# Kernel tuning notes

Hardware: AMD Instinct MI355X
Metric: run time of the kernel (lower is better)

## Reference

```python
import jax, jax.numpy as jnp
import numpy as np

D0, D1 = 512, 512          # PSF / sensor dims (DIMS0, DIMS1)
P0, P1 = D0 // 2, D1 // 2  # pad sizes
ITERS = 20
MU1, MU2, MU3 = 1e-6, 1e-5, 1e-5
TAU = 1e-4 * 1000.0        # 0.1, as in module


def _ct(x):  # zero-pad crop-adjoint: sensor -> full size
    return jnp.pad(x, [(0, 0)] * (x.ndim - 2) + [(P0, P0), (P1, P1)])


def _c(x):  # crop full -> sensor size
    return x[..., P0:P0 + D0, P1:P1 + D1]


def _fft2(x):
    return jnp.fft.fft2(x, axes=(-2, -1))


def _ifft2(x):
    return jnp.fft.ifft2(x, axes=(-2, -1))


def _ifftshift(x):
    return jnp.fft.ifftshift(x, axes=(-2, -1))


def _fftshift(x):
    return jnp.fft.fftshift(x, axes=(-2, -1))


def _H(x, Hf):  # forward blur operator
    return jnp.real(_fftshift(_ifft2(Hf * _fft2(_ifftshift(x)))))


def _Hadj(x, Hf):  # adjoint blur operator
    return jnp.real(_fftshift(_ifft2(jnp.conj(Hf) * _fft2(_ifftshift(x)))))


def _psi(x):  # finite differences stacked on last axis -> (..., 2)
    return jnp.stack([jnp.roll(x, 1, axis=-2) - x,
                      jnp.roll(x, 1, axis=-1) - x], axis=-1)


def _psit(u):  # adjoint of _psi
    d0, d1 = u[..., 0], u[..., 1]
    return (jnp.roll(d0, -1, axis=-2) - d0) + (jnp.roll(d1, -1, axis=-1) - d1)


def _soft(v, thresh):
    return jnp.sign(v) * jnp.maximum(jnp.abs(v) - thresh, 0.0)


def _make_ltl():  # FFT of laplacian kernel (Psi^T Psi in Fourier domain)
    lapl = np.zeros((2 * D0, 2 * D1), np.float32)
    lapl[0, 0] = 4.0
    lapl[0, 1] = -1.0
    lapl[1, 0] = -1.0
    lapl[0, -1] = -1.0
    lapl[-1, 0] = -1.0
    return jnp.fft.fft2(jnp.asarray(lapl))


def setup_inputs() -> dict:
    key = jax.random.key(0)
    k1, k2 = jax.random.split(key)
    y = jax.random.uniform(k1, (8, 1, D0, D1), dtype=jnp.float32)
    h = jax.random.uniform(k2, (D0, D1), dtype=jnp.float32)
    return {"y": y, "h": h}


def reference(y, h):
    Hf = _fft2(_ifftshift(_ct(h[None])))            # (1, 2D0, 2D1) complex
    LtL = _make_ltl()                               # (2D0, 2D1) complex
    Vdiv = 1.0 / (_ct(jnp.ones((1, 1, D0, D1), y.dtype)) + MU1)
    Rdiv = 1.0 / (MU1 * jnp.abs(jnp.conj(Hf) * Hf) + MU2 * jnp.abs(LtL) + MU3)
    CTy = _ct(y)                                    # (B,1,2D0,2D1)

    B = y.shape[0]
    full = (B, 1, 2 * D0, 2 * D1)
    X = jnp.zeros(full, y.dtype)
    U = jnp.zeros(full + (2,), y.dtype)
    V = jnp.zeros(full, y.dtype)
    W = jnp.zeros(full, y.dtype)
    a1 = jnp.zeros(full, y.dtype)
    a2 = jnp.zeros(full + (2,), y.dtype)
    a3 = jnp.zeros(full, y.dtype)

    def step(carry, _):
        X, U, V, W, a1, a2, a3 = carry
        U = _soft(_psi(X) + a2 / MU2, TAU / MU2)
        V = Vdiv * (a1 + MU1 * _H(X, Hf) + CTy)
        W = jnp.maximum(a3 / MU3 + X, 0.0)
        r = (MU3 * W - a3) + _psit(MU2 * U - a2) + _Hadj(MU1 * V - a1, Hf)
        X = jnp.real(_fftshift(_ifft2(Rdiv * _fft2(_ifftshift(r)))))
        a1 = a1 + MU1 * (_H(X, Hf) - V)
        a2 = a2 + MU2 * (_psi(X) - U)
        a3 = a3 + MU3 * (X - W)
        return (X, U, V, W, a1, a2, a3), None

    (X, _, _, _, _, _, _), _ = jax.lax.scan(step, (X, U, V, W, a1, a2, a3), None, length=ITERS)
    return _c(X)
```

## Files before the change

kernel.cpp:

```cpp
#include <hip/hip_runtime.h>
#include <math.h>

#define N 1024
#define NN (1024*1024)
#define BATCH 8

static constexpr float MU1 = 1e-6f, MU2 = 1e-5f, MU3 = 1e-5f;

__device__ __forceinline__ float2 cmulf(float2 a, float2 b){
  return make_float2(a.x*b.x - a.y*b.y, a.x*b.y + a.y*b.x);
}
__device__ __forceinline__ float2 conjf(float2 a){ return make_float2(a.x, -a.y); }
__device__ __forceinline__ float softf(float v, float T){
  float a = fmaxf(fabsf(v) - T, 0.f);
  return copysignf(a, v);
}
__device__ __forceinline__ int rev4_10(int p){
  return ((p&3)<<8) | (((p>>2)&3)<<6) | (((p>>4)&3)<<4) | (((p>>6)&3)<<2) | ((p>>8)&3);
}
__device__ __forceinline__ int foldc(int k){
  if (k == 0) return 0;
  if (k == 512) return 1;
  return (k < 512) ? 2*k : 2*(1024-k)+1;
}
__device__ __forceinline__ int unfoldc(int c){
  if (c < 2) return c ? 512 : 0;
  return (c & 1) ? 1024 - ((c-1)>>1) : (c>>1);
}

#define BF4F(x0,x1,x2,x3,u0,u1,u2,u3) { \
  float2 t02p = make_float2((x0).x+(x2).x, (x0).y+(x2).y); \
  float2 t02m = make_float2((x0).x-(x2).x, (x0).y-(x2).y); \
  float2 t13p = make_float2((x1).x+(x3).x, (x1).y+(x3).y); \
  float2 t13m = make_float2((x1).x-(x3).x, (x1).y-(x3).y); \
  u0 = make_float2(t02p.x+t13p.x, t02p.y+t13p.y); \
  u2 = make_float2(t02p.x-t13p.x, t02p.y-t13p.y); \
  u1 = make_float2(t02m.x+t13m.y, t02m.y-t13m.x); \
  u3 = make_float2(t02m.x-t13m.y, t02m.y+t13m.x); }
#define BF4I(x0,x1,x2,x3,u0,u1,u2,u3) { \
  float2 t02p = make_float2((x0).x+(x2).x, (x0).y+(x2).y); \
  float2 t02m = make_float2((x0).x-(x2).x, (x0).y-(x2).y); \
  float2 t13p = make_float2((x1).x+(x3).x, (x1).y+(x3).y); \
  float2 t13m = make_float2((x1).x-(x3).x, (x1).y-(x3).y); \
  u0 = make_float2(t02p.x+t13p.x, t02p.y+t13p.y); \
  u2 = make_float2(t02p.x-t13p.x, t02p.y-t13p.y); \
  u1 = make_float2(t02m.x-t13m.y, t02m.y+t13m.x); \
  u3 = make_float2(t02m.x+t13m.y, t02m.y-t13m.x); }

template<int DIR>
__device__ __forceinline__ void fft1024(float2* bufA, float2* bufB,
                                        const float2* Ws, int tid){
  float2* cur = bufA; float2* oth = bufB;
  int s = 1;
  for (int st = 0; st < 10; ++st){
    int m = 512 >> st;
    #pragma unroll
    for (int bb = 0; bb < 2; ++bb){
      int b = tid + bb*256;
      int p = b >> st;
      int q = b & (s-1);
      float2 a = cur[b];
      float2 c = cur[b + 512];
      float2 w = Ws[b & ~(s-1)];
      if (DIR > 0) w.y = -w.y;
      float2 d = make_float2(a.x - c.x, a.y - c.y);
      oth[q + s*(2*p)]   = make_float2(a.x + c.x, a.y + c.y);
      oth[q + s*(2*p+1)] = cmulf(d, w);
    }
    __syncthreads();
    float2* t = cur; cur = oth; oth = t;
    s <<= 1;
  }
}

__global__ void k_twiddle(float2* W){
  int j = blockIdx.x*blockDim.x + threadIdx.x;
  if (j < 768){
    double a = -2.0 * M_PI * (double)j / 1024.0;
    W[j] = make_float2((float)cos(a), (float)sin(a));
  }
}

__global__ void k_build_h(const float* __restrict__ h, float2* __restrict__ Z){
  int idx = blockIdx.x*256 + threadIdx.x;
  int i = idx >> 10, j = idx & 1023;
  float v = 0.f;
  if (i >= 256 && i < 768 && j >= 256 && j < 768)
    v = h[(i-256)*512 + (j-256)];
  Z[idx] = make_float2(v, 0.f);
}

__global__ void k_filters2(const float2* __restrict__ ZT, float2* __restrict__ HfCb,
                           float* __restrict__ RdCb){
  int id = blockIdx.x*256 + threadIdx.x;
  int blk = id >> 13;
  int rem = id & 8191;
  int p = rem >> 3, c = rem & 7;
  int colp = (blk << 3) | c;
  int ki = rev4_10(p);
  int kj = unfoldc(colp);
  float2 v = ZT[((size_t)kj << 10) | (size_t)ki];
  float sgn = ((ki + kj) & 1) ? -1.f : 1.f;
  HfCb[id] = make_float2(sgn*v.x, sgn*v.y);
  double mag2 = (double)v.x*(double)v.x + (double)v.y*(double)v.y;
  double ltl = 4.0 - 2.0*cos(2.0*M_PI*(double)ki/1024.0)
                   - 2.0*cos(2.0*M_PI*(double)kj/1024.0);
  double rd = 1.0 / ((double)MU1*mag2 + (double)MU2*ltl + (double)MU3);
  RdCb[id] = (float)(rd / ((double)N * (double)N));
}

__global__ void k_init(float* __restrict__ X, float* __restrict__ G1,
                       float* __restrict__ K, float* __restrict__ M,
                       float* __restrict__ G0a, float* __restrict__ G0b,
                       const float* __restrict__ y){
  int idx = blockIdx.x*256 + threadIdx.x;
  int e = idx >> 20, r = (idx >> 10) & 1023, c = idx & 1023;
  X[idx] = 0.f; G1[idx] = 0.f; K[idx] = 0.f; G0a[idx] = 0.f; G0b[idx] = 0.f;
  float m = 0.f;
  if (r >= 256 && r < 768 && c >= 256 && c < 768)
    m = y[(size_t)e*262144 + (size_t)(r-256)*512 + (c-256)] * (MU1/(1.f + MU1));
  M[idx] = m;
}

__global__ __launch_bounds__(256) void k_pA(const float* __restrict__ X,
                                            const float* __restrict__ G0r,
                                            float* __restrict__ G0w,
                                            const float* __restrict__ G1,
                                            const float* __restrict__ K,
                                            const float* __restrict__ M,
                                            float2* __restrict__ Z,
                                            const float2* __restrict__ Wg, int e0){
  __shared__ float2 bufA[N], bufB[N], Ws[512];
  int tid = threadIdx.x;
  int bid = blockIdx.x;
  int i = ((bid & 7) << 7) + (bid >> 3);
  int ce = blockIdx.y, e = e0 + ce;
  size_t eb  = (size_t)e*NN;
  size_t rb  = eb + (size_t)i*N;
  size_t rbm = eb + (size_t)((i-1)&1023)*N;
  size_t rbp = eb + (size_t)((i+1)&1023)*N;
  size_t zb  = (size_t)ce*NN + (size_t)i*N;
  for (int k = tid; k < 512; k += 256) Ws[k] = Wg[k];
  const float T = 1e4f;
  for (int j = tid; j < N; j += 256){
    float xm = X[rbm+j], x = X[rb+j], xp = X[rbp+j];
    float psi0  = xm - x;
    float psi0p = x - xp;
    float g0  = G0r[rb+j], g0p = G0r[rbp+j];
    float u0  = softf(2.f*psi0  - g0 *(1.f/MU2), T);
    float u0p = softf(2.f*psi0p - g0p*(1.f/MU2), T);
    float g0n  = MU2*(u0  - psi0 ) + g0;
    float g0np = MU2*(u0p - psi0p) + g0p;
    G0w[rb+j] = g0n;
    int jp = (j+1) & 1023;
    float s = K[rb+j] + (g0np - g0n) + (G1[rb+jp] - G1[rb+j]);
    bufA[j] = make_float2(s, M[rb+j]);
  }
  __syncthreads();
  fft1024<-1>(bufA, bufB, Ws, tid);
  for (int j = tid; j < N; j += 256) bufB[foldc(j)] = bufA[j];
  __syncthreads();
  for (int j = tid; j < N; j += 256) Z[zb+j] = bufB[j];
}

template<int DIR>
__global__ __launch_bounds__(256) void k_fft_row(float2* Z, const float2* __restrict__ Wg){
  __shared__ float2 bufA[N], bufB[N], Ws[512];
  int tid = threadIdx.x;
  size_t base = ((size_t)blockIdx.y * N + blockIdx.x) * N;
  for (int k = tid; k < 512; k += 256) Ws[k] = Wg[k];
  for (int k = tid; k < N; k += 256) bufA[k] = Z[base + k];
  __syncthreads();
  fft1024<DIR>(bufA, bufB, Ws, tid);
  for (int k = tid; k < N; k += 256) Z[base + k] = bufA[k];
}

__global__ void k_transpose_ip(float2* Z){
  __shared__ float2 ta[32][33], tb[32][33];
  int t = blockIdx.x, ti = 0;
  while (t >= 32 - ti){ t -= 32 - ti; ti++; }
  int tj = ti + t;
  size_t base = (size_t)blockIdx.y * NN;
  int ra = ti*32, ca = tj*32;
  for (int k = threadIdx.y; k < 32; k += 8){
    ta[k][threadIdx.x] = Z[base + (size_t)(ra+k)*N + ca + threadIdx.x];
    if (ti != tj)
      tb[k][threadIdx.x] = Z[base + (size_t)(ca+k)*N + ra + threadIdx.x];
  }
  __syncthreads();
  for (int k = threadIdx.y; k < 32; k += 8){
    Z[base + (size_t)(ra+k)*N + ca + threadIdx.x] = (ti!=tj) ? tb[threadIdx.x][k]
                                                             : ta[threadIdx.x][k];
    if (ti != tj)
      Z[base + (size_t)(ca+k)*N + ra + threadIdx.x] = ta[threadIdx.x][k];
  }
}

#define TADDR(r,c) ((((r)*9) + (c)) ^ (((r) & 16) >> 1))
#define CPV 512
__global__ __launch_bounds__(CPV, 4) void k_colpass(float2* __restrict__ Z,
    const float2* __restrict__ HfCb, const float* __restrict__ RdCb,
    const float2* __restrict__ Wg){
  __shared__ float2 tile[9216];
  __shared__ float2 Ws[768];
  int tid = threadIdx.x;
  int blk = blockIdx.x;
  size_t zbase = (size_t)blockIdx.y*NN + ((size_t)blk<<3);
  for (int k = tid; k < 768; k += CPV) Ws[k] = Wg[k];
  for (int k = tid; k < 8192; k += CPV){
    int r = k >> 3, c = k & 7;
    tile[TADDR(r,c)] = Z[zbase + (size_t)r*N + c];
  }
  __syncthreads();
  {
    int c = tid & 7, j2 = tid >> 3;
    float2 v[4][4];
    #pragma unroll
    for (int a = 0; a < 4; ++a)
      #pragma unroll
      for (int b = 0; b < 4; ++b)
        v[a][b] = tile[TADDR(j2 + 64*b + 256*a, c)];
    #pragma unroll
    for (int b = 0; b < 4; ++b){
      int j1 = j2 + 64*b;
      float2 u0,u1,u2,u3;
      BF4F(v[0][b],v[1][b],v[2][b],v[3][b],u0,u1,u2,u3);
      v[0][b] = u0;
      v[1][b] = cmulf(u1, Ws[j1]);
      v[2][b] = cmulf(u2, Ws[2*j1]);
      v[3][b] = cmulf(u3, Ws[3*j1]);
    }
    int tw = j2 << 2;
    #pragma unroll
    for (int a = 0; a < 4; ++a){
      float2 u0,u1,u2,u3;
      BF4F(v[a][0],v[a][1],v[a][2],v[a][3],u0,u1,u2,u3);
      tile[TADDR(j2 + 256*a, c)]       = u0;
      tile[TADDR(j2 + 64 + 256*a, c)]  = cmulf(u1, Ws[tw]);
      tile[TADDR(j2 + 128 + 256*a, c)] = cmulf(u2, Ws[2*tw]);
      tile[TADDR(j2 + 192 + 256*a, c)] = cmulf(u3, Ws[3*tw]);
    }
  }
  __syncthreads();
  {
    int c = tid & 7, vv = tid >> 3;
    int B2 = vv >> 2, j2 = vv & 3;
    int r0 = 64*B2 + j2;
    float2 v[4][4];
    #pragma unroll
    for (int a = 0; a < 4; ++a)
      #pragma unroll
      for (int b = 0; b < 4; ++b)
        v[a][b] = tile[TADDR(r0 + 4*b + 16*a, c)];
    #pragma unroll
    for (int b = 0; b < 4; ++b){
      int tw = (j2 + 4*b) << 4;
      float2 u0,u1,u2,u3;
      BF4F(v[0][b],v[1][b],v[2][b],v[3][b],u0,u1,u2,u3);
      v[0][b] = u0;
      v[1][b] = cmulf(u1, Ws[tw]);
      v[2][b] = cmulf(u2, Ws[2*tw]);
      v[3][b] = cmulf(u3, Ws[3*tw]);
    }
    int tw3 = j2 << 6;
    #pragma unroll
    for (int a = 0; a < 4; ++a){
      float2 u0,u1,u2,u3;
      BF4F(v[a][0],v[a][1],v[a][2],v[a][3],u0,u1,u2,u3);
      tile[TADDR(r0 + 16*a, c)]      = u0;
      tile[TADDR(r0 + 16*a + 4, c)]  = cmulf(u1, Ws[tw3]);
      tile[TADDR(r0 + 16*a + 8, c)]  = cmulf(u2, Ws[2*tw3]);
      tile[TADDR(r0 + 16*a + 12, c)] = cmulf(u3, Ws[3*tw3]);
    }
  }
  __syncthreads();
  for (int k = tid; k < 2048; k += CPV){
    int c = k & 7, t = k >> 3;
    int r = 4*t;
    float2 x0 = tile[TADDR(r,c)],   x1 = tile[TADDR(r+1,c)];
    float2 x2 = tile[TADDR(r+2,c)], x3 = tile[TADDR(r+3,c)];
    float2 u0,u1,u2,u3;
    BF4F(x0,x1,x2,x3,u0,u1,u2,u3);
    tile[TADDR(r,c)] = u0; tile[TADDR(r+1,c)] = u1;
    tile[TADDR(r+2,c)] = u2; tile[TADDR(r+3,c)] = u3;
  }
  __syncthreads();
  {
    size_t fbase = (size_t)blk << 13;
    for (int k = tid; k < 8192; k += CPV){
      int p = k >> 3, c = k & 7;
      int k1 = rev4_10(p);
      int q = rev4_10((1024 - k1) & 1023);
      int colp = (blk << 3) + c;
      int cm = (colp < 2) ? c : (c ^ 1);
      int pid = (q << 3) | cm;
      if (pid < k) continue;
      float2 Zk = tile[TADDR(p,c)];
      float2 Zr = tile[TADDR(q,cm)];
      float Sre = 0.5f*(Zk.x + Zr.x);
      float Sim = 0.5f*(Zk.y - Zr.y);
      float Mre = 0.5f*(Zk.y + Zr.y);
      float Mim = 0.5f*(Zr.x - Zk.x);
      float2 hf = HfCb[fbase + k];
      float rd  = RdCb[fbase + k];
      float fr = rd*(Sre + hf.x*Mre + hf.y*Mim);
      float fi = rd*(Sim + hf.x*Mim - hf.y*Mre);
      float hr = hf.x*fr - hf.y*fi;
      float hi = hf.x*fi + hf.y*fr;
      tile[TADDR(p,c)] = make_float2(fr - hi, fi + hr);
      if (pid != k) tile[TADDR(q,cm)] = make_float2(fr + hi, hr - fi);
    }
  }
  __syncthreads();
  {
    int c = tid & 7, G = tid >> 3;
    int r0 = 16*G;
    float2 v[4][4];
    #pragma unroll
    for (int a = 0; a < 4; ++a)
      #pragma unroll
      for (int b = 0; b < 4; ++b)
        v[a][b] = tile[TADDR(r0 + 4*a + b, c)];
    #pragma unroll
    for (int a = 0; a < 4; ++a){
      float2 u0,u1,u2,u3;
      BF4I(v[a][0],v[a][1],v[a][2],v[a][3],u0,u1,u2,u3);
      v[a][0]=u0; v[a][1]=u1; v[a][2]=u2; v[a][3]=u3;
    }
    #pragma unroll
    for (int b = 0; b < 4; ++b){
      int tw = b << 6;
      float2 x0 = v[0][b];
      float2 x1 = cmulf(v[1][b], conjf(Ws[tw]));
      float2 x2 = cmulf(v[2][b], conjf(Ws[2*tw]));
      float2 x3 = cmulf(v[3][b], conjf(Ws[3*tw]));
      float2 u0,u1,u2,u3;
      BF4I(x0,x1,x2,x3,u0,u1,u2,u3);
      tile[TADDR(r0 + b, c)]      = u0;
      tile[TADDR(r0 + 4 + b, c)]  = u1;
      tile[TADDR(r0 + 8 + b, c)]  = u2;
      tile[TADDR(r0 + 12 + b, c)] = u3;
    }
  }
  __syncthreads();
  {
    int c = tid & 7, vv = tid >> 3;
    int T3 = vv >> 4, jj = vv & 15;
    int r0 = 256*T3 + jj;
    float2 v[4][4];
    #pragma unroll
    for (int a = 0; a < 4; ++a)
      #pragma unroll
      for (int b = 0; b < 4; ++b)
        v[a][b] = tile[TADDR(r0 + 16*a + 64*b, c)];
    int tw2 = jj << 4;
    #pragma unroll
    for (int b = 0; b < 4; ++b){
      float2 x0 = v[0][b];
      float2 x1 = cmulf(v[1][b], conjf(Ws[tw2]));
      float2 x2 = cmulf(v[2][b], conjf(Ws[2*tw2]));
      float2 x3 = cmulf(v[3][b], conjf(Ws[3*tw2]));
      float2 u0,u1,u2,u3;
      BF4I(x0,x1,x2,x3,u0,u1,u2,u3);
      v[0][b]=u0; v[1][b]=u1; v[2][b]=u2; v[3][b]=u3;
    }
    #pragma unroll
    for (int a = 0; a < 4; ++a){
      int tw = (jj + 16*a) << 2;
      float2 x0 = v[a][0];
      float2 x1 = cmulf(v[a][1], conjf(Ws[tw]));
      float2 x2 = cmulf(v[a][2], conjf(Ws[2*tw]));
      float2 x3 = cmulf(v[a][3], conjf(Ws[3*tw]));
      float2 u0,u1,u2,u3;
      BF4I(x0,x1,x2,x3,u0,u1,u2,u3);
      tile[TADDR(r0 + 16*a, c)]       = u0;
      tile[TADDR(r0 + 16*a + 64, c)]  = u1;
      tile[TADDR(r0 + 16*a + 128, c)] = u2;
      tile[TADDR(r0 + 16*a + 192, c)] = u3;
    }
  }
  __syncthreads();
  for (int k = tid; k < 2048; k += CPV){
    int c = k & 7, t = k >> 3;
    float2 x0 = tile[TADDR(t,c)];
    float2 x1 = cmulf(tile[TADDR(t+256,c)], conjf(Ws[t]));
    float2 x2 = cmulf(tile[TADDR(t+512,c)], conjf(Ws[2*t]));
    float2 x3 = cmulf(tile[TADDR(t+768,c)], conjf(Ws[3*t]));
    float2 u0,u1,u2,u3;
    BF4I(x0,x1,x2,x3,u0,u1,u2,u3);
    tile[TADDR(t,c)] = u0;     tile[TADDR(t+256,c)] = u1;
    tile[TADDR(t+512,c)] = u2; tile[TADDR(t+768,c)] = u3;
  }
  __syncthreads();
  for (int k = tid; k < 8192; k += CPV){
    int r = k >> 3, c = k & 7;
    Z[zbase + (size_t)r*N + c] = tile[TADDR(r,c)];
  }
}

__global__ __launch_bounds__(256) void k_p5(const float2* __restrict__ Z,
                                            float* __restrict__ X, float* __restrict__ K,
                                            float* __restrict__ M, float* __restrict__ G1,
                                            const float* __restrict__ y,
                                            float* __restrict__ out, int writeOut,
                                            const float2* __restrict__ Wg, int e0){
  __shared__ float2 bufA[N], bufB[N], Ws[512];
  int tid = threadIdx.x;
  int i = blockIdx.x, ce = blockIdx.y, e = e0 + ce;
  size_t zb = (size_t)ce*NN + (size_t)i*N;
  size_t sb = (size_t)e*NN + (size_t)i*N;
  for (int k = tid; k < 512; k += 256) Ws[k] = Wg[k];
  for (int k = tid; k < N; k += 256) bufB[k] = Z[zb + k];
  __syncthreads();
  for (int k = tid; k < N; k += 256) bufA[k] = bufB[foldc(k)];
  __syncthreads();
  fft1024<1>(bufA, bufB, Ws, tid);
  bool rcent = (i >= 256 && i < 768);
  const float T = 1e4f;
  for (int j = tid; j < N; j += 256){
    float x = bufA[j].x, hx = bufA[j].y;
    X[sb+j] = x;
    float kk = K[sb+j];
    float w = fmaxf(2.f*x - kk*(1.f/MU3), 0.f);
    K[sb+j] = MU3*(w - x) + kk;
    float m = M[sb+j];
    bool cent = rcent && (j >= 256 && j < 768);
    float cty  = cent ? y[(size_t)e*262144 + (size_t)(i-256)*512 + (j-256)] : 0.f;
    float vdiv = cent ? (1.f/(1.f + MU1)) : (1.f/MU1);
    float v = vdiv*(2.f*MU1*hx - m + cty);
    M[sb+j] = MU1*(v - hx) + m;
    float xm = bufA[(j-1)&1023].x;
    float psi1 = xm - x;
    float g1 = G1[sb+j];
    float u1 = softf(2.f*psi1 - g1*(1.f/MU2), T);
    G1[sb+j] = MU2*(u1 - psi1) + g1;
    if (writeOut && cent)
      out[(size_t)e*262144 + (size_t)(i-256)*512 + (j-256)] = x;
  }
}

__global__ void k_crop(const float* __restrict__ X, float* __restrict__ out){
  int t = blockIdx.x*256 + threadIdx.x;
  int e = t >> 18;
  int r = (t >> 9) & 511;
  int c = t & 511;
  out[t] = X[(size_t)e*NN + (size_t)(r+256)*N + (c+256)];
}

extern "C" void kernel_launch(void* const* d_in, const int* in_sizes, int n_in,
                              void* d_out, int out_size, void* d_ws, size_t ws_size,
                              hipStream_t stream){
  const float* y = (const float*)d_in[0];
  const float* h = (const float*)d_in[1];
  float* out = (float*)d_out;

  size_t fplane = (size_t)BATCH * NN;
  float* X   = (float*)d_ws;
  float* G1  = X   + fplane;
  float* K   = G1  + fplane;
  float* M   = K   + fplane;
  float* G0a = M   + fplane;
  float* G0b = G0a + fplane;
  float2* HfCb = (float2*)(G0b + fplane);
  float*  RdCb = (float*)(HfCb + NN);
  float2* Wtab = (float2*)(RdCb + NN);
  float2* Zws  = Wtab + 768;
  size_t used = (size_t)((char*)Zws - (char*)d_ws);

  int CH = 0;
  for (int c = BATCH; c >= 1; c >>= 1)
    if (used + (size_t)c * NN * sizeof(float2) <= ws_size){ CH = c; break; }
  bool fallback = (CH == 0);
  float2* Z = fallback ? (float2*)d_out : Zws;
  if (CH == 0) CH = 1;

  k_twiddle<<<3, 256, 0, stream>>>(Wtab);
  k_build_h<<<NN/256, 256, 0, stream>>>(h, Z);
  k_fft_row<-1><<<dim3(N,1), 256, 0, stream>>>(Z, Wtab);
  k_transpose_ip<<<dim3(528,1), dim3(32,8), 0, stream>>>(Z);
  k_fft_row<-1><<<dim3(N,1), 256, 0, stream>>>(Z, Wtab);
  k_filters2<<<NN/256, 256, 0, stream>>>(Z, HfCb, RdCb);
  k_init<<<BATCH*NN/256, 256, 0, stream>>>(X, G1, K, M, G0a, G0b, y);

  for (int t = 0; t < 20; ++t){
    const float* G0r = (t & 1) ? G0b : G0a;
    float*       G0w = (t & 1) ? G0a : G0b;
    int wo = (t == 19 && !fallback) ? 1 : 0;
    for (int e0 = 0; e0 < BATCH; e0 += CH){
      k_pA<<<dim3(N,CH), 256, 0, stream>>>(X, G0r, G0w, G1, K, M, Z, Wtab, e0);
      k_colpass<<<dim3(128,CH), CPV, 0, stream>>>(Z, HfCb, RdCb, Wtab);
      k_p5<<<dim3(N,CH), 256, 0, stream>>>(Z, X, K, M, G1, y, out, wo, Wtab, e0);
    }
  }
  if (fallback)
    k_crop<<<(BATCH*512*512)/256, 256, 0, stream>>>(X, out);
}
```

Measured before the change: 3.769 ms.

## Process four rows per block with register-blocked radix-4 row FFTs

Replaces the per-row radix-2 shared-memory FFT in the two row-pass kernels with a batched radix-4 (16-point register block) FFT over four rows per block, using a swizzled shared tile. The output is written directly in the digit-reversed, folded order the column pass expects. This cuts the number of barrier-separated stages and the shared-memory round trips, and launches a quarter as many blocks. The K (W/a3) update also moves from the last pass into the first one, so K is read and written once per element in a single place. The larger shared footprint may lower occupancy.

Result: slower. 4.246 ms (+12.7%).

```diff
diff --git a/kernel.cpp b/kernel.cpp
--- a/kernel.cpp
+++ b/kernel.cpp
@@ -73,6 +73,166 @@
   }
 }
 
+#define RA(p,r) (((((p)<<2)|(r))) ^ ((((p)>>2)&3)<<2))
+
+__device__ __forceinline__ void fwd_r4(float2* tile, const float2* Ws, int tid){
+  int row = tid & 3, g = tid >> 2;
+  {
+    int j2 = g;
+    float2 v[4][4];
+    #pragma unroll
+    for (int a = 0; a < 4; ++a)
+      #pragma unroll
+      for (int b = 0; b < 4; ++b)
+        v[a][b] = tile[RA(j2 + 64*b + 256*a, row)];
+    #pragma unroll
+    for (int b = 0; b < 4; ++b){
+      int j1 = j2 + 64*b;
+      float2 u0,u1,u2,u3;
+      BF4F(v[0][b],v[1][b],v[2][b],v[3][b],u0,u1,u2,u3);
+      v[0][b] = u0;
+      v[1][b] = cmulf(u1, Ws[j1]);
+      v[2][b] = cmulf(u2, Ws[2*j1]);
+      v[3][b] = cmulf(u3, Ws[3*j1]);
+    }
+    int tw = j2 << 2;
+    #pragma unroll
+    for (int a = 0; a < 4; ++a){
+      float2 u0,u1,u2,u3;
+      BF4F(v[a][0],v[a][1],v[a][2],v[a][3],u0,u1,u2,u3);
+      tile[RA(j2 + 256*a, row)]       = u0;
+      tile[RA(j2 + 64 + 256*a, row)]  = cmulf(u1, Ws[tw]);
+      tile[RA(j2 + 128 + 256*a, row)] = cmulf(u2, Ws[2*tw]);
+      tile[RA(j2 + 192 + 256*a, row)] = cmulf(u3, Ws[3*tw]);
+    }
+  }
+  __syncthreads();
+  {
+    int B2 = g >> 2, j2 = g & 3;
+    int r0 = 64*B2 + j2;
+    float2 v[4][4];
+    #pragma unroll
+    for (int a = 0; a < 4; ++a)
+      #pragma unroll
+      for (int b = 0; b < 4; ++b)
+        v[a][b] = tile[RA(r0 + 4*b + 16*a, row)];
+    #pragma unroll
+    for (int b = 0; b < 4; ++b){
+      int tw = (j2 + 4*b) << 4;
+      float2 u0,u1,u2,u3;
+      BF4F(v[0][b],v[1][b],v[2][b],v[3][b],u0,u1,u2,u3);
+      v[0][b] = u0;
+      v[1][b] = cmulf(u1, Ws[tw]);
+      v[2][b] = cmulf(u2, Ws[2*tw]);
+      v[3][b] = cmulf(u3, Ws[3*tw]);
+    }
+    int tw3 = j2 << 6;
+    #pragma unroll
+    for (int a = 0; a < 4; ++a){
+      float2 u0,u1,u2,u3;
+      BF4F(v[a][0],v[a][1],v[a][2],v[a][3],u0,u1,u2,u3);
+      tile[RA(r0 + 16*a, row)]      = u0;
+      tile[RA(r0 + 16*a + 4, row)]  = cmulf(u1, Ws[tw3]);
+      tile[RA(r0 + 16*a + 8, row)]  = cmulf(u2, Ws[2*tw3]);
+      tile[RA(r0 + 16*a + 12, row)] = cmulf(u3, Ws[3*tw3]);
+    }
+  }
+  __syncthreads();
+  for (int k = tid; k < 1024; k += 256){
+    int r2 = k & 3, t = k >> 2;
+    int p = 4*t;
+    float2 x0 = tile[RA(p,r2)],   x1 = tile[RA(p+1,r2)];
+    float2 x2 = tile[RA(p+2,r2)], x3 = tile[RA(p+3,r2)];
+    float2 u0,u1,u2,u3;
+    BF4F(x0,x1,x2,x3,u0,u1,u2,u3);
+    tile[RA(p,r2)] = u0;   tile[RA(p+1,r2)] = u1;
+    tile[RA(p+2,r2)] = u2; tile[RA(p+3,r2)] = u3;
+  }
+  __syncthreads();
+}
+
+__device__ __forceinline__ void inv_r4(float2* tile, const float2* Ws, int tid){
+  int row = tid & 3, g = tid >> 2;
+  {
+    int r0 = 16*g;
+    float2 v[4][4];
+    #pragma unroll
+    for (int a = 0; a < 4; ++a)
+      #pragma unroll
+      for (int b = 0; b < 4; ++b)
+        v[a][b] = tile[RA(r0 + 4*a + b, row)];
+    #pragma unroll
+    for (int a = 0; a < 4; ++a){
+      float2 u0,u1,u2,u3;
+      BF4I(v[a][0],v[a][1],v[a][2],v[a][3],u0,u1,u2,u3);
+      v[a][0]=u0; v[a][1]=u1; v[a][2]=u2; v[a][3]=u3;
+    }
+    #pragma unroll
+    for (int b = 0; b < 4; ++b){
+      int tw = b << 6;
+      float2 x0 = v[0][b];
+      float2 x1 = cmulf(v[1][b], conjf(Ws[tw]));
+      float2 x2 = cmulf(v[2][b], conjf(Ws[2*tw]));
+      float2 x3 = cmulf(v[3][b], conjf(Ws[3*tw]));
+      float2 u0,u1,u2,u3;
+      BF4I(x0,x1,x2,x3,u0,u1,u2,u3);
+      tile[RA(r0 + b, row)]      = u0;
+      tile[RA(r0 + 4 + b, row)]  = u1;
+      tile[RA(r0 + 8 + b, row)]  = u2;
+      tile[RA(r0 + 12 + b, row)] = u3;
+    }
+  }
+  __syncthreads();
+  {
+    int T3 = g >> 4, jj = g & 15;
+    int r0 = 256*T3 + jj;
+    float2 v[4][4];
+    #pragma unroll
+    for (int a = 0; a < 4; ++a)
+      #pragma unroll
+      for (int b = 0; b < 4; ++b)
+        v[a][b] = tile[RA(r0 + 16*a + 64*b, row)];
+    int tw2 = jj << 4;
+    #pragma unroll
+    for (int b = 0; b < 4; ++b){
+      float2 x0 = v[0][b];
+      float2 x1 = cmulf(v[1][b], conjf(Ws[tw2]));
+      float2 x2 = cmulf(v[2][b], conjf(Ws[2*tw2]));
+      float2 x3 = cmulf(v[3][b], conjf(Ws[3*tw2]));
+      float2 u0,u1,u2,u3;
+      BF4I(x0,x1,x2,x3,u0,u1,u2,u3);
+      v[0][b]=u0; v[1][b]=u1; v[2][b]=u2; v[3][b]=u3;
+    }
+    #pragma unroll
+    for (int a = 0; a < 4; ++a){
+      int tw = (jj + 16*a) << 2;
+      float2 x0 = v[a][0];
+      float2 x1 = cmulf(v[a][1], conjf(Ws[tw]));
+      float2 x2 = cmulf(v[a][2], conjf(Ws[2*tw]));
+      float2 x3 = cmulf(v[a][3], conjf(Ws[3*tw]));
+      float2 u0,u1,u2,u3;
+      BF4I(x0,x1,x2,x3,u0,u1,u2,u3);
+      tile[RA(r0 + 16*a, row)]       = u0;
+      tile[RA(r0 + 16*a + 64, row)]  = u1;
+      tile[RA(r0 + 16*a + 128, row)] = u2;
+      tile[RA(r0 + 16*a + 192, row)] = u3;
+    }
+  }
+  __syncthreads();
+  for (int k = tid; k < 1024; k += 256){
+    int r2 = k & 3, t = k >> 2;
+    float2 x0 = tile[RA(t,r2)];
+    float2 x1 = cmulf(tile[RA(t+256,r2)], conjf(Ws[t]));
+    float2 x2 = cmulf(tile[RA(t+512,r2)], conjf(Ws[2*t]));
+    float2 x3 = cmulf(tile[RA(t+768,r2)], conjf(Ws[3*t]));
+    float2 u0,u1,u2,u3;
+    BF4I(x0,x1,x2,x3,u0,u1,u2,u3);
+    tile[RA(t,r2)] = u0;     tile[RA(t+256,r2)] = u1;
+    tile[RA(t+512,r2)] = u2; tile[RA(t+768,r2)] = u3;
+  }
+  __syncthreads();
+}
+
 __global__ void k_twiddle(float2* W){
   int j = blockIdx.x*blockDim.x + threadIdx.x;
   if (j < 768){
@@ -126,41 +286,52 @@
                                             const float* __restrict__ G0r,
                                             float* __restrict__ G0w,
                                             const float* __restrict__ G1,
-                                            const float* __restrict__ K,
+                                            float* __restrict__ K,
                                             const float* __restrict__ M,
                                             float2* __restrict__ Z,
                                             const float2* __restrict__ Wg, int e0){
-  __shared__ float2 bufA[N], bufB[N], Ws[512];
+  __shared__ float2 tile[4096];
+  __shared__ float2 Ws[768];
   int tid = threadIdx.x;
   int bid = blockIdx.x;
-  int i = ((bid & 7) << 7) + (bid >> 3);
+  int i0 = 4 * (((bid & 7) << 5) | (bid >> 3));
   int ce = blockIdx.y, e = e0 + ce;
-  size_t eb  = (size_t)e*NN;
-  size_t rb  = eb + (size_t)i*N;
-  size_t rbm = eb + (size_t)((i-1)&1023)*N;
-  size_t rbp = eb + (size_t)((i+1)&1023)*N;
-  size_t zb  = (size_t)ce*NN + (size_t)i*N;
-  for (int k = tid; k < 512; k += 256) Ws[k] = Wg[k];
+  size_t eb = (size_t)e*NN;
+  for (int k = tid; k < 768; k += 256) Ws[k] = Wg[k];
   const float T = 1e4f;
-  for (int j = tid; j < N; j += 256){
-    float xm = X[rbm+j], x = X[rb+j], xp = X[rbp+j];
-    float psi0  = xm - x;
-    float psi0p = x - xp;
-    float g0  = G0r[rb+j], g0p = G0r[rbp+j];
-    float u0  = softf(2.f*psi0  - g0 *(1.f/MU2), T);
-    float u0p = softf(2.f*psi0p - g0p*(1.f/MU2), T);
-    float g0n  = MU2*(u0  - psi0 ) + g0;
-    float g0np = MU2*(u0p - psi0p) + g0p;
-    G0w[rb+j] = g0n;
-    int jp = (j+1) & 1023;
-    float s = K[rb+j] + (g0np - g0n) + (G1[rb+jp] - G1[rb+j]);
-    bufA[j] = make_float2(s, M[rb+j]);
-  }
-  __syncthreads();
-  fft1024<-1>(bufA, bufB, Ws, tid);
-  for (int j = tid; j < N; j += 256) bufB[foldc(j)] = bufA[j];
-  __syncthreads();
-  for (int j = tid; j < N; j += 256) Z[zb+j] = bufB[j];
+  for (int r = 0; r < 4; ++r){
+    int i = i0 + r;
+    size_t rb  = eb + (size_t)i*N;
+    size_t rbm = eb + (size_t)((i-1)&1023)*N;
+    size_t rbp = eb + (size_t)((i+1)&1023)*N;
+    for (int j = tid; j < N; j += 256){
+      float xm = X[rbm+j], x = X[rb+j], xp = X[rbp+j];
+      float psi0  = xm - x;
+      float psi0p = x - xp;
+      float g0  = G0r[rb+j], g0p = G0r[rbp+j];
+      float u0  = softf(2.f*psi0  - g0 *(1.f/MU2), T);
+      float u0p = softf(2.f*psi0p - g0p*(1.f/MU2), T);
+      float g0n  = MU2*(u0  - psi0 ) + g0;
+      float g0np = MU2*(u0p - psi0p) + g0p;
+      G0w[rb+j] = g0n;
+      float kk = K[rb+j];
+      float w  = fmaxf(2.f*x - kk*(1.f/MU3), 0.f);
+      float kn = MU3*(w - x) + kk;
+      K[rb+j] = kn;
+      int jp = (j+1) & 1023;
+      float s = kn + (g0np - g0n) + (G1[rb+jp] - G1[rb+j]);
+      tile[RA(j,r)] = make_float2(s, M[rb+j]);
+    }
+  }
+  __syncthreads();
+  fwd_r4(tile, Ws, tid);
+  for (int r = 0; r < 4; ++r){
+    size_t zb = (size_t)ce*NN + (size_t)(i0+r)*N;
+    for (int c = tid; c < N; c += 256){
+      int pos = rev4_10(unfoldc(c));
+      Z[zb + c] = tile[RA(pos, r)];
+    }
+  }
 }
 
 template<int DIR>
@@ -399,43 +570,50 @@
 }
 
 __global__ __launch_bounds__(256) void k_p5(const float2* __restrict__ Z,
-                                            float* __restrict__ X, float* __restrict__ K,
+                                            float* __restrict__ X,
                                             float* __restrict__ M, float* __restrict__ G1,
                                             const float* __restrict__ y,
                                             float* __restrict__ out, int writeOut,
                                             const float2* __restrict__ Wg, int e0){
-  __shared__ float2 bufA[N], bufB[N], Ws[512];
+  __shared__ float2 tile[4096];
+  __shared__ float2 Ws[768];
   int tid = threadIdx.x;
-  int i = blockIdx.x, ce = blockIdx.y, e = e0 + ce;
-  size_t zb = (size_t)ce*NN + (size_t)i*N;
-  size_t sb = (size_t)e*NN + (size_t)i*N;
-  for (int k = tid; k < 512; k += 256) Ws[k] = Wg[k];
-  for (int k = tid; k < N; k += 256) bufB[k] = Z[zb + k];
-  __syncthreads();
-  for (int k = tid; k < N; k += 256) bufA[k] = bufB[foldc(k)];
-  __syncthreads();
-  fft1024<1>(bufA, bufB, Ws, tid);
-  bool rcent = (i >= 256 && i < 768);
+  int bid = blockIdx.x;
+  int i0 = 4 * (((bid & 7) << 5) | (bid >> 3));
+  int ce = blockIdx.y, e = e0 + ce;
+  for (int k = tid; k < 768; k += 256) Ws[k] = Wg[k];
+  for (int r = 0; r < 4; ++r){
+    size_t zb = (size_t)ce*NN + (size_t)(i0+r)*N;
+    for (int c = tid; c < N; c += 256){
+      int pos = rev4_10(unfoldc(c));
+      tile[RA(pos, r)] = Z[zb + c];
+    }
+  }
+  __syncthreads();
+  inv_r4(tile, Ws, tid);
   const float T = 1e4f;
-  for (int j = tid; j < N; j += 256){
-    float x = bufA[j].x, hx = bufA[j].y;
-    X[sb+j] = x;
-    float kk = K[sb+j];
-    float w = fmaxf(2.f*x - kk*(1.f/MU3), 0.f);
-    K[sb+j] = MU3*(w - x) + kk;
-    float m = M[sb+j];
-    bool cent = rcent && (j >= 256 && j < 768);
-    float cty  = cent ? y[(size_t)e*262144 + (size_t)(i-256)*512 + (j-256)] : 0.f;
-    float vdiv = cent ? (1.f/(1.f + MU1)) : (1.f/MU1);
-    float v = vdiv*(2.f*MU1*hx - m + cty);
-    M[sb+j] = MU1*(v - hx) + m;
-    float xm = bufA[(j-1)&1023].x;
-    float psi1 = xm - x;
-    float g1 = G1[sb+j];
-    float u1 = softf(2.f*psi1 - g1*(1.f/MU2), T);
-    G1[sb+j] = MU2*(u1 - psi1) + g1;
-    if (writeOut && cent)
-      out[(size_t)e*262144 + (size_t)(i-256)*512 + (j-256)] = x;
+  for (int r = 0; r < 4; ++r){
+    int i = i0 + r;
+    size_t sb = (size_t)e*NN + (size_t)i*N;
+    bool rcent = (i >= 256 && i < 768);
+    for (int j = tid; j < N; j += 256){
+      float2 xv = tile[RA(j, r)];
+      float x = xv.x, hx = xv.y;
+      X[sb+j] = x;
+      float m = M[sb+j];
+      bool cent = rcent && (j >= 256 && j < 768);
+      float cty  = cent ? y[(size_t)e*262144 + (size_t)(i-256)*512 + (j-256)] : 0.f;
+      float vdiv = cent ? (1.f/(1.f + MU1)) : (1.f/MU1);
+      float v = vdiv*(2.f*MU1*hx - m + cty);
+      M[sb+j] = MU1*(v - hx) + m;
+      float xm = tile[RA((j-1)&1023, r)].x;
+      float psi1 = xm - x;
+      float g1 = G1[sb+j];
+      float u1 = softf(2.f*psi1 - g1*(1.f/MU2), T);
+      G1[sb+j] = MU2*(u1 - psi1) + g1;
+      if (writeOut && cent)
+        out[(size_t)e*262144 + (size_t)(i-256)*512 + (j-256)] = x;
+    }
   }
 }
 
@@ -487,9 +665,9 @@
     float*       G0w = (t & 1) ? G0a : G0b;
     int wo = (t == 19 && !fallback) ? 1 : 0;
     for (int e0 = 0; e0 < BATCH; e0 += CH){
-      k_pA<<<dim3(N,CH), 256, 0, stream>>>(X, G0r, G0w, G1, K, M, Z, Wtab, e0);
+      k_pA<<<dim3(256,CH), 256, 0, stream>>>(X, G0r, G0w, G1, K, M, Z, Wtab, e0);
       k_colpass<<<dim3(128,CH), CPV, 0, stream>>>(Z, HfCb, RdCb, Wtab);
-      k_p5<<<dim3(N,CH), 256, 0, stream>>>(Z, X, K, M, G1, y, out, wo, Wtab, e0);
+      k_p5<<<dim3(256,CH), 256, 0, stream>>>(Z, X, M, G1, y, out, wo, Wtab, e0);
     }
   }
   if (fallback)
```

## Drop init kernel via first-iteration modes and narrow column-pass tiles to four columns

Applied to the files above, without the earlier changes.

Removes the state-zeroing init kernel. Iteration 0 now synthesizes its inputs in-kernel: X=0 means only M is nonzero, computed directly from y. Iteration 1 treats the unwritten G0 buffer as zero, which skips several full-size reads and writes. The column-pass kernel is also reworked to handle 4 columns per block with 256 threads and a new padded LDS layout. That doubles the grid and halves shared memory per block for better occupancy, but uses narrower 4-element global row segments, which may coalesce less well.

After: 4.149 ms. +10.1%, slower.

```diff
diff --git a/kernel.cpp b/kernel.cpp
--- a/kernel.cpp
+++ b/kernel.cpp
@@ -93,10 +93,10 @@
 __global__ void k_filters2(const float2* __restrict__ ZT, float2* __restrict__ HfCb,
                            float* __restrict__ RdCb){
   int id = blockIdx.x*256 + threadIdx.x;
-  int blk = id >> 13;
-  int rem = id & 8191;
-  int p = rem >> 3, c = rem & 7;
-  int colp = (blk << 3) | c;
+  int blk = id >> 12;
+  int rem = id & 4095;
+  int p = rem >> 2, c = rem & 3;
+  int colp = (blk << 2) | c;
   int ki = rev4_10(p);
   int kj = unfoldc(colp);
   float2 v = ZT[((size_t)kj << 10) | (size_t)ki];
@@ -109,27 +109,16 @@
   RdCb[id] = (float)(rd / ((double)N * (double)N));
 }
 
-__global__ void k_init(float* __restrict__ X, float* __restrict__ G1,
-                       float* __restrict__ K, float* __restrict__ M,
-                       float* __restrict__ G0a, float* __restrict__ G0b,
-                       const float* __restrict__ y){
-  int idx = blockIdx.x*256 + threadIdx.x;
-  int e = idx >> 20, r = (idx >> 10) & 1023, c = idx & 1023;
-  X[idx] = 0.f; G1[idx] = 0.f; K[idx] = 0.f; G0a[idx] = 0.f; G0b[idx] = 0.f;
-  float m = 0.f;
-  if (r >= 256 && r < 768 && c >= 256 && c < 768)
-    m = y[(size_t)e*262144 + (size_t)(r-256)*512 + (c-256)] * (MU1/(1.f + MU1));
-  M[idx] = m;
-}
-
 __global__ __launch_bounds__(256) void k_pA(const float* __restrict__ X,
                                             const float* __restrict__ G0r,
                                             float* __restrict__ G0w,
                                             const float* __restrict__ G1,
                                             const float* __restrict__ K,
                                             const float* __restrict__ M,
+                                            const float* __restrict__ y,
                                             float2* __restrict__ Z,
-                                            const float2* __restrict__ Wg, int e0){
+                                            const float2* __restrict__ Wg,
+                                            int e0, int mode){
   __shared__ float2 bufA[N], bufB[N], Ws[512];
   int tid = threadIdx.x;
   int bid = blockIdx.x;
@@ -142,19 +131,30 @@
   size_t zb  = (size_t)ce*NN + (size_t)i*N;
   for (int k = tid; k < 512; k += 256) Ws[k] = Wg[k];
   const float T = 1e4f;
-  for (int j = tid; j < N; j += 256){
-    float xm = X[rbm+j], x = X[rb+j], xp = X[rbp+j];
-    float psi0  = xm - x;
-    float psi0p = x - xp;
-    float g0  = G0r[rb+j], g0p = G0r[rbp+j];
-    float u0  = softf(2.f*psi0  - g0 *(1.f/MU2), T);
-    float u0p = softf(2.f*psi0p - g0p*(1.f/MU2), T);
-    float g0n  = MU2*(u0  - psi0 ) + g0;
-    float g0np = MU2*(u0p - psi0p) + g0p;
-    G0w[rb+j] = g0n;
-    int jp = (j+1) & 1023;
-    float s = K[rb+j] + (g0np - g0n) + (G1[rb+jp] - G1[rb+j]);
-    bufA[j] = make_float2(s, M[rb+j]);
+  if (mode == 2){
+    bool rcent = (i >= 256 && i < 768);
+    for (int j = tid; j < N; j += 256){
+      float m0 = 0.f;
+      if (rcent && j >= 256 && j < 768)
+        m0 = y[(size_t)e*262144 + (size_t)(i-256)*512 + (j-256)] * (MU1/(1.f + MU1));
+      bufA[j] = make_float2(0.f, m0);
+    }
+  } else {
+    for (int j = tid; j < N; j += 256){
+      float xm = X[rbm+j], x = X[rb+j], xp = X[rbp+j];
+      float psi0  = xm - x;
+      float psi0p = x - xp;
+      float g0  = (mode == 1) ? 0.f : G0r[rb+j];
+      float g0p = (mode == 1) ? 0.f : G0r[rbp+j];
+      float u0  = softf(2.f*psi0  - g0 *(1.f/MU2), T);
+      float u0p = softf(2.f*psi0p - g0p*(1.f/MU2), T);
+      float g0n  = MU2*(u0  - psi0 ) + g0;
+      float g0np = MU2*(u0p - psi0p) + g0p;
+      G0w[rb+j] = g0n;
+      int jp = (j+1) & 1023;
+      float s = K[rb+j] + (g0np - g0n) + (G1[rb+jp] - G1[rb+j]);
+      bufA[j] = make_float2(s, M[rb+j]);
+    }
   }
   __syncthreads();
   fft1024<-1>(bufA, bufB, Ws, tid);
@@ -196,30 +196,29 @@
   }
 }
 
-#define TADDR(r,c) ((((r)*9) + (c)) ^ (((r) & 16) >> 1))
-#define CPV 512
-__global__ __launch_bounds__(CPV, 4) void k_colpass(float2* __restrict__ Z,
+#define RA4(p,c) ((((p)<<2)) + (c) + ((p)>>2))
+__global__ __launch_bounds__(256, 4) void k_colpass(float2* __restrict__ Z,
     const float2* __restrict__ HfCb, const float* __restrict__ RdCb,
     const float2* __restrict__ Wg){
-  __shared__ float2 tile[9216];
+  __shared__ float2 tile[4352];
   __shared__ float2 Ws[768];
   int tid = threadIdx.x;
   int blk = blockIdx.x;
-  size_t zbase = (size_t)blockIdx.y*NN + ((size_t)blk<<3);
-  for (int k = tid; k < 768; k += CPV) Ws[k] = Wg[k];
-  for (int k = tid; k < 8192; k += CPV){
-    int r = k >> 3, c = k & 7;
-    tile[TADDR(r,c)] = Z[zbase + (size_t)r*N + c];
+  size_t zbase = (size_t)blockIdx.y*NN + ((size_t)blk<<2);
+  for (int k = tid; k < 768; k += 256) Ws[k] = Wg[k];
+  for (int k = tid; k < 4096; k += 256){
+    int r = k >> 2, c = k & 3;
+    tile[RA4(r,c)] = Z[zbase + (size_t)r*N + c];
   }
   __syncthreads();
   {
-    int c = tid & 7, j2 = tid >> 3;
+    int c = tid & 3, j2 = tid >> 2;
     float2 v[4][4];
     #pragma unroll
     for (int a = 0; a < 4; ++a)
       #pragma unroll
       for (int b = 0; b < 4; ++b)
-        v[a][b] = tile[TADDR(j2 + 64*b + 256*a, c)];
+        v[a][b] = tile[RA4(j2 + 64*b + 256*a, c)];
     #pragma unroll
     for (int b = 0; b < 4; ++b){
       int j1 = j2 + 64*b;
@@ -235,15 +234,15 @@
     for (int a = 0; a < 4; ++a){
       float2 u0,u1,u2,u3;
       BF4F(v[a][0],v[a][1],v[a][2],v[a][3],u0,u1,u2,u3);
-      tile[TADDR(j2 + 256*a, c)]       = u0;
-      tile[TADDR(j2 + 64 + 256*a, c)]  = cmulf(u1, Ws[tw]);
-      tile[TADDR(j2 + 128 + 256*a, c)] = cmulf(u2, Ws[2*tw]);
-      tile[TADDR(j2 + 192 + 256*a, c)] = cmulf(u3, Ws[3*tw]);
+      tile[RA4(j2 + 256*a, c)]       = u0;
+      tile[RA4(j2 + 64 + 256*a, c)]  = cmulf(u1, Ws[tw]);
+      tile[RA4(j2 + 128 + 256*a, c)] = cmulf(u2, Ws[2*tw]);
+      tile[RA4(j2 + 192 + 256*a, c)] = cmulf(u3, Ws[3*tw]);
     }
   }
   __syncthreads();
   {
-    int c = tid & 7, vv = tid >> 3;
+    int c = tid & 3, vv = tid >> 2;
     int B2 = vv >> 2, j2 = vv & 3;
     int r0 = 64*B2 + j2;
     float2 v[4][4];
@@ -251,7 +250,7 @@
     for (int a = 0; a < 4; ++a)
       #pragma unroll
       for (int b = 0; b < 4; ++b)
-        v[a][b] = tile[TADDR(r0 + 4*b + 16*a, c)];
+        v[a][b] = tile[RA4(r0 + 4*b + 16*a, c)];
     #pragma unroll
     for (int b = 0; b < 4; ++b){
       int tw = (j2 + 4*b) << 4;
@@ -267,36 +266,36 @@
     for (int a = 0; a < 4; ++a){
       float2 u0,u1,u2,u3;
       BF4F(v[a][0],v[a][1],v[a][2],v[a][3],u0,u1,u2,u3);
-      tile[TADDR(r0 + 16*a, c)]      = u0;
-      tile[TADDR(r0 + 16*a + 4, c)]  = cmulf(u1, Ws[tw3]);
-      tile[TADDR(r0 + 16*a + 8, c)]  = cmulf(u2, Ws[2*tw3]);
-      tile[TADDR(r0 + 16*a + 12, c)] = cmulf(u3, Ws[3*tw3]);
-    }
-  }
-  __syncthreads();
-  for (int k = tid; k < 2048; k += CPV){
-    int c = k & 7, t = k >> 3;
+      tile[RA4(r0 + 16*a, c)]      = u0;
+      tile[RA4(r0 + 16*a + 4, c)]  = cmulf(u1, Ws[tw3]);
+      tile[RA4(r0 + 16*a + 8, c)]  = cmulf(u2, Ws[2*tw3]);
+      tile[RA4(r0 + 16*a + 12, c)] = cmulf(u3, Ws[3*tw3]);
+    }
+  }
+  __syncthreads();
+  for (int k = tid; k < 1024; k += 256){
+    int c = k & 3, t = k >> 2;
     int r = 4*t;
-    float2 x0 = tile[TADDR(r,c)],   x1 = tile[TADDR(r+1,c)];
-    float2 x2 = tile[TADDR(r+2,c)], x3 = tile[TADDR(r+3,c)];
+    float2 x0 = tile[RA4(r,c)],   x1 = tile[RA4(r+1,c)];
+    float2 x2 = tile[RA4(r+2,c)], x3 = tile[RA4(r+3,c)];
     float2 u0,u1,u2,u3;
     BF4F(x0,x1,x2,x3,u0,u1,u2,u3);
-    tile[TADDR(r,c)] = u0; tile[TADDR(r+1,c)] = u1;
-    tile[TADDR(r+2,c)] = u2; tile[TADDR(r+3,c)] = u3;
+    tile[RA4(r,c)] = u0; tile[RA4(r+1,c)] = u1;
+    tile[RA4(r+2,c)] = u2; tile[RA4(r+3,c)] = u3;
   }
   __syncthreads();
   {
-    size_t fbase = (size_t)blk << 13;
-    for (int k = tid; k < 8192; k += CPV){
-      int p = k >> 3, c = k & 7;
+    size_t fbase = (size_t)blk << 12;
+    for (int k = tid; k < 4096; k += 256){
+      int p = k >> 2, c = k & 3;
       int k1 = rev4_10(p);
       int q = rev4_10((1024 - k1) & 1023);
-      int colp = (blk << 3) + c;
+      int colp = (blk << 2) + c;
       int cm = (colp < 2) ? c : (c ^ 1);
-      int pid = (q << 3) | cm;
+      int pid = (q << 2) | cm;
       if (pid < k) continue;
-      float2 Zk = tile[TADDR(p,c)];
-      float2 Zr = tile[TADDR(q,cm)];
+      float2 Zk = tile[RA4(p,c)];
+      float2 Zr = tile[RA4(q,cm)];
       float Sre = 0.5f*(Zk.x + Zr.x);
       float Sim = 0.5f*(Zk.y - Zr.y);
       float Mre = 0.5f*(Zk.y + Zr.y);
@@ -307,20 +306,20 @@
       float fi = rd*(Sim + hf.x*Mim - hf.y*Mre);
       float hr = hf.x*fr - hf.y*fi;
       float hi = hf.x*fi + hf.y*fr;
-      tile[TADDR(p,c)] = make_float2(fr - hi, fi + hr);
-      if (pid != k) tile[TADDR(q,cm)] = make_float2(fr + hi, hr - fi);
+      tile[RA4(p,c)] = make_float2(fr - hi, fi + hr);
+      if (pid != k) tile[RA4(q,cm)] = make_float2(fr + hi, hr - fi);
     }
   }
   __syncthreads();
   {
-    int c = tid & 7, G = tid >> 3;
+    int c = tid & 3, G = tid >> 2;
     int r0 = 16*G;
     float2 v[4][4];
     #pragma unroll
     for (int a = 0; a < 4; ++a)
       #pragma unroll
       for (int b = 0; b < 4; ++b)
-        v[a][b] = tile[TADDR(r0 + 4*a + b, c)];
+        v[a][b] = tile[RA4(r0 + 4*a + b, c)];
     #pragma unroll
     for (int a = 0; a < 4; ++a){
       float2 u0,u1,u2,u3;
@@ -336,15 +335,15 @@
       float2 x3 = cmulf(v[3][b], conjf(Ws[3*tw]));
       float2 u0,u1,u2,u3;
       BF4I(x0,x1,x2,x3,u0,u1,u2,u3);
-      tile[TADDR(r0 + b, c)]      = u0;
-      tile[TADDR(r0 + 4 + b, c)]  = u1;
-      tile[TADDR(r0 + 8 + b, c)]  = u2;
-      tile[TADDR(r0 + 12 + b, c)] = u3;
+      tile[RA4(r0 + b, c)]      = u0;
+      tile[RA4(r0 + 4 + b, c)]  = u1;
+      tile[RA4(r0 + 8 + b, c)]  = u2;
+      tile[RA4(r0 + 12 + b, c)] = u3;
     }
   }
   __syncthreads();
   {
-    int c = tid & 7, vv = tid >> 3;
+    int c = tid & 3, vv = tid >> 2;
     int T3 = vv >> 4, jj = vv & 15;
     int r0 = 256*T3 + jj;
     float2 v[4][4];
@@ -352,7 +351,7 @@
     for (int a = 0; a < 4; ++a)
       #pragma unroll
       for (int b = 0; b < 4; ++b)
-        v[a][b] = tile[TADDR(r0 + 16*a + 64*b, c)];
+        v[a][b] = tile[RA4(r0 + 16*a + 64*b, c)];
     int tw2 = jj << 4;
     #pragma unroll
     for (int b = 0; b < 4; ++b){
@@ -373,28 +372,28 @@
       float2 x3 = cmulf(v[a][3], conjf(Ws[3*tw]));
       float2 u0,u1,u2,u3;
       BF4I(x0,x1,x2,x3,u0,u1,u2,u3);
-      tile[TADDR(r0 + 16*a, c)]       = u0;
-      tile[TADDR(r0 + 16*a + 64, c)]  = u1;
-      tile[TADDR(r0 + 16*a + 128, c)] = u2;
-      tile[TADDR(r0 + 16*a + 192, c)] = u3;
-    }
-  }
-  __syncthreads();
-  for (int k = tid; k < 2048; k += CPV){
-    int c = k & 7, t = k >> 3;
-    float2 x0 = tile[TADDR(t,c)];
-    float2 x1 = cmulf(tile[TADDR(t+256,c)], conjf(Ws[t]));
-    float2 x2 = cmulf(tile[TADDR(t+512,c)], conjf(Ws[2*t]));
-    float2 x3 = cmulf(tile[TADDR(t+768,c)], conjf(Ws[3*t]));
+      tile[RA4(r0 + 16*a, c)]       = u0;
+      tile[RA4(r0 + 16*a + 64, c)]  = u1;
+      tile[RA4(r0 + 16*a + 128, c)] = u2;
+      tile[RA4(r0 + 16*a + 192, c)] = u3;
+    }
+  }
+  __syncthreads();
+  for (int k = tid; k < 1024; k += 256){
+    int c = k & 3, t = k >> 2;
+    float2 x0 = tile[RA4(t,c)];
+    float2 x1 = cmulf(tile[RA4(t+256,c)], conjf(Ws[t]));
+    float2 x2 = cmulf(tile[RA4(t+512,c)], conjf(Ws[2*t]));
+    float2 x3 = cmulf(tile[RA4(t+768,c)], conjf(Ws[3*t]));
     float2 u0,u1,u2,u3;
     BF4I(x0,x1,x2,x3,u0,u1,u2,u3);
-    tile[TADDR(t,c)] = u0;     tile[TADDR(t+256,c)] = u1;
-    tile[TADDR(t+512,c)] = u2; tile[TADDR(t+768,c)] = u3;
-  }
-  __syncthreads();
-  for (int k = tid; k < 8192; k += CPV){
-    int r = k >> 3, c = k & 7;
-    Z[zbase + (size_t)r*N + c] = tile[TADDR(r,c)];
+    tile[RA4(t,c)] = u0;     tile[RA4(t+256,c)] = u1;
+    tile[RA4(t+512,c)] = u2; tile[RA4(t+768,c)] = u3;
+  }
+  __syncthreads();
+  for (int k = tid; k < 4096; k += 256){
+    int r = k >> 2, c = k & 3;
+    Z[zbase + (size_t)r*N + c] = tile[RA4(r,c)];
   }
 }
 
@@ -403,7 +402,8 @@
                                             float* __restrict__ M, float* __restrict__ G1,
                                             const float* __restrict__ y,
                                             float* __restrict__ out, int writeOut,
-                                            const float2* __restrict__ Wg, int e0){
+                                            const float2* __restrict__ Wg, int e0,
+                                            int first){
   __shared__ float2 bufA[N], bufB[N], Ws[512];
   int tid = threadIdx.x;
   int i = blockIdx.x, ce = blockIdx.y, e = e0 + ce;
@@ -420,18 +420,18 @@
   for (int j = tid; j < N; j += 256){
     float x = bufA[j].x, hx = bufA[j].y;
     X[sb+j] = x;
-    float kk = K[sb+j];
+    bool cent = rcent && (j >= 256 && j < 768);
+    float cty  = cent ? y[(size_t)e*262144 + (size_t)(i-256)*512 + (j-256)] : 0.f;
+    float kk = first ? 0.f : K[sb+j];
     float w = fmaxf(2.f*x - kk*(1.f/MU3), 0.f);
     K[sb+j] = MU3*(w - x) + kk;
-    float m = M[sb+j];
-    bool cent = rcent && (j >= 256 && j < 768);
-    float cty  = cent ? y[(size_t)e*262144 + (size_t)(i-256)*512 + (j-256)] : 0.f;
+    float m = first ? (cent ? cty*(MU1/(1.f+MU1)) : 0.f) : M[sb+j];
     float vdiv = cent ? (1.f/(1.f + MU1)) : (1.f/MU1);
     float v = vdiv*(2.f*MU1*hx - m + cty);
     M[sb+j] = MU1*(v - hx) + m;
     float xm = bufA[(j-1)&1023].x;
     float psi1 = xm - x;
-    float g1 = G1[sb+j];
+    float g1 = first ? 0.f : G1[sb+j];
     float u1 = softf(2.f*psi1 - g1*(1.f/MU2), T);
     G1[sb+j] = MU2*(u1 - psi1) + g1;
     if (writeOut && cent)
@@ -480,16 +480,16 @@
   k_transpose_ip<<<dim3(528,1), dim3(32,8), 0, stream>>>(Z);
   k_fft_row<-1><<<dim3(N,1), 256, 0, stream>>>(Z, Wtab);
   k_filters2<<<NN/256, 256, 0, stream>>>(Z, HfCb, RdCb);
-  k_init<<<BATCH*NN/256, 256, 0, stream>>>(X, G1, K, M, G0a, G0b, y);
 
   for (int t = 0; t < 20; ++t){
     const float* G0r = (t & 1) ? G0b : G0a;
     float*       G0w = (t & 1) ? G0a : G0b;
+    int mode = (t == 0) ? 2 : ((t == 1) ? 1 : 0);
     int wo = (t == 19 && !fallback) ? 1 : 0;
     for (int e0 = 0; e0 < BATCH; e0 += CH){
-      k_pA<<<dim3(N,CH), 256, 0, stream>>>(X, G0r, G0w, G1, K, M, Z, Wtab, e0);
-      k_colpass<<<dim3(128,CH), CPV, 0, stream>>>(Z, HfCb, RdCb, Wtab);
-      k_p5<<<dim3(N,CH), 256, 0, stream>>>(Z, X, K, M, G1, y, out, wo, Wtab, e0);
+      k_pA<<<dim3(N,CH), 256, 0, stream>>>(X, G0r, G0w, G1, K, M, y, Z, Wtab, e0, mode);
+      k_colpass<<<dim3(256,CH), 256, 0, stream>>>(Z, HfCb, RdCb, Wtab);
+      k_p5<<<dim3(N,CH), 256, 0, stream>>>(Z, X, K, M, G1, y, out, wo, Wtab, e0, (t==0)?1:0);
     }
   }
   if (fallback)
```
